# Performance work log

Hardware: AMD Instinct MI355X
Metric: run time of the kernel (lower is better)

The kernel has to match this reference:

```python
import jax, jax.numpy as jnp
import numpy as np

B, L, H, N = 8, 2048, 512, 64  # batch, seq_len, d_model, SSM state size


def setup_inputs() -> dict:
    key = jax.random.key(0)
    ks = jax.random.split(key, 10)
    x = jax.random.normal(ks[0], (B, L, H), jnp.float32)
    # S4D-style parameters (diagonal SSM, S4D-Lin init)
    log_dt = jnp.log(1e-3) + jax.random.uniform(ks[1], (H,), jnp.float32) * (jnp.log(1e-1) - jnp.log(1e-3))
    A_re = -0.5 * jnp.ones((H, N), jnp.float32)
    A_im = jnp.tile(np.pi * jnp.arange(N, dtype=np.float32), (H, 1))
    C_re = jax.random.normal(ks[2], (H, N), jnp.float32) * (0.5 ** 0.5)
    C_im = jax.random.normal(ks[3], (H, N), jnp.float32) * (0.5 ** 0.5)
    D_skip = jax.random.normal(ks[4], (H,), jnp.float32)
    # S4 output linear (GLU): d_model -> 2*d_model, then gated
    W_out = jax.random.normal(ks[5], (2 * H, H), jnp.float32) / np.sqrt(H)
    b_out = jnp.zeros((2 * H,), jnp.float32)
    # LayerNorms
    g1 = jnp.ones((H,), jnp.float32); beta1 = jnp.zeros((H,), jnp.float32)
    g2 = jnp.ones((H,), jnp.float32); beta2 = jnp.zeros((H,), jnp.float32)
    # 1x1 conv FFN (kernel_size=1 => pointwise linear), d_ff = d_model
    W1 = jax.random.normal(ks[6], (H, H), jnp.float32) / np.sqrt(H)
    bc1 = jnp.zeros((H,), jnp.float32)
    W2 = jax.random.normal(ks[7], (H, H), jnp.float32) / np.sqrt(H)
    bc2 = jnp.zeros((H,), jnp.float32)
    return dict(x=x, log_dt=log_dt, A_re=A_re, A_im=A_im, C_re=C_re, C_im=C_im,
                D_skip=D_skip, W_out=W_out, b_out=b_out, g1=g1, beta1=beta1,
                g2=g2, beta2=beta2, W1=W1, bc1=bc1, W2=W2, bc2=bc2)


def _layer_norm(x, g, b):
    mu = jnp.mean(x, axis=-1, keepdims=True)
    var = jnp.mean((x - mu) ** 2, axis=-1, keepdims=True)
    return (x - mu) / jnp.sqrt(var + 1e-5) * g + b


def _s4(x, log_dt, A_re, A_im, C_re, C_im, D_skip, W_out, b_out):
    # x: (B, L, H) channels-last (transposed=False)
    Lx = x.shape[1]
    dt = jnp.exp(log_dt)                       # (H,)
    A = A_re + 1j * A_im                       # (H, N) diagonal state matrix
    dtA = A * dt[:, None]
    # ZOH discretization of C: Ct = C * (exp(dt*A) - 1) / A
    Ct = (C_re + 1j * C_im) * ((jnp.exp(dtA) - 1.0) / A)
    # Vandermonde kernel: K[h, l] = 2 Re sum_n Ct[h,n] exp(dt*A[h,n]*l)
    l = jnp.arange(Lx, dtype=jnp.float32)
    K = 2.0 * jnp.real(jnp.einsum('hn,hnl->hl', Ct, jnp.exp(dtA[:, :, None] * l)))
    # FFT long convolution (linear conv via zero-padded circular conv)
    u = jnp.swapaxes(x, 1, 2)                  # (B, H, L)
    n = 2 * Lx
    y = jnp.fft.irfft(jnp.fft.rfft(u, n) * jnp.fft.rfft(K, n)[None], n)[..., :Lx]
    y = y + D_skip[None, :, None] * u          # skip connection D*u
    y = jax.nn.gelu(y)                         # S4 default activation
    # output linear + GLU (S4 default postact)
    z = jnp.einsum('bhl,fh->bfl', y, W_out) + b_out[None, :, None]
    a, g = jnp.split(z, 2, axis=1)
    y = a * jax.nn.sigmoid(g)
    return jnp.swapaxes(y, 1, 2)               # (B, L, H)


def reference(x, log_dt, A_re, A_im, C_re, C_im, D_skip, W_out, b_out,
              g1, beta1, g2, beta2, W1, bc1, W2, bc2):
    new_x = _s4(x, log_dt, A_re, A_im, C_re, C_im, D_skip, W_out, b_out)
    x = x + new_x
    x = _layer_norm(x, g1, beta1)
    # FFN via 1x1 convs (pointwise linears); dropout is identity in eval
    y = jax.nn.relu(jnp.einsum('blh,fh->blf', x, W1) + bc1)
    y = jnp.einsum('blf,hf->blh', y, W2) + bc2
    return _layer_norm(x + y, g2, beta2)
```

## Files before the change

kernel.cpp:

```cpp
#include <hip/hip_runtime.h>
#include <cstddef>
#include <cstdint>

#define B_DIM 8
#define L_DIM 2048
#define H_DIM 512
#define N_DIM 64
#define HN (H_DIM * N_DIM)
#define BLH (B_DIM * L_DIM * H_DIM)
#define M_DIM (B_DIM * L_DIM)

typedef unsigned short u16;
typedef short bf16x8 __attribute__((ext_vector_type(8)));
typedef float floatx4 __attribute__((ext_vector_type(4)));

__device__ __forceinline__ float sigmoidf_(float v) {
    return 1.0f / (1.0f + __expf(-v));
}

__device__ __forceinline__ float gelu_tanh_(float x) {
    float x3 = x * x * x;
    float z = 0.7978845608028654f * fmaf(0.044715f, x3, x);
    float e = __expf(-2.0f * fabsf(z));
    float th = (1.0f - e) / (1.0f + e);
    th = copysignf(th, z);
    return 0.5f * x * (1.0f + th);
}

__device__ __forceinline__ u16 f2b(float f) {
    unsigned u = __float_as_uint(f);
    unsigned r = (u + 0x7fffu + ((u >> 16) & 1u)) >> 16;
    return (u16)r;
}
__device__ __forceinline__ float b2f(u16 u) {
    return __uint_as_float(((unsigned)u) << 16);
}
__device__ __forceinline__ void unpack2(unsigned u, float& a, float& b) {
    a = __uint_as_float(u << 16);
    b = __uint_as_float(u & 0xffff0000u);
}
__device__ __forceinline__ unsigned pack2(float a, float b) {
    return (unsigned)f2b(a) | ((unsigned)f2b(b) << 16);
}

__device__ __forceinline__ void csq(float& r, float& i) {
    float nr = r * r - i * i;
    i = 2.0f * r * i;
    r = nr;
}

__global__ __launch_bounds__(256) void setup_kernel(
    const float* __restrict__ x, const float* __restrict__ W_out,
    const float* __restrict__ W1, const float* __restrict__ W2,
    const float* __restrict__ log_dt, const float* __restrict__ A_re,
    const float* __restrict__ A_im, const float* __restrict__ C_re,
    const float* __restrict__ C_im, const float* __restrict__ g1,
    const float* __restrict__ beta1,
    u16* __restrict__ XT, u16* __restrict__ Wobf, u16* __restrict__ W1gbf,
    u16* __restrict__ W2bf, float* __restrict__ P, u16* __restrict__ Toep_bf,
    float* __restrict__ c1, float* __restrict__ c2)
{
    __shared__ float tile[32][33];
    __shared__ float ktab_s[4][64];
    const int bid = blockIdx.x;
    const int t   = threadIdx.x;

    if (bid < 8192) {
        int b  = bid >> 10;
        int hy = (bid >> 6) & 15;
        int lx = bid & 63;
        int l0 = lx * 32, h0 = hy * 32;
        int tx = t & 31, ty = t >> 5;
        #pragma unroll
        for (int r = 0; r < 4; ++r)
            tile[ty + r * 8][tx] = x[((size_t)b * L_DIM + l0 + ty + r * 8) * H_DIM + h0 + tx];
        __syncthreads();
        #pragma unroll
        for (int r = 0; r < 4; ++r)
            XT[(((size_t)b * H_DIM + h0 + ty + r * 8) << 11) + l0 + tx] = f2b(tile[tx][ty + r * 8]);
    } else if (bid < 9216) {
        int off = bid - 8192;
        if (off < 512) {
            int i = off * 256 + t;
            float4 v = *(const float4*)(W_out + (size_t)i * 4);
            uint2 p; p.x = pack2(v.x, v.y); p.y = pack2(v.z, v.w);
            *(uint2*)(Wobf + (size_t)i * 4) = p;
        } else if (off < 768) {
            int i = (off - 512) * 256 + t;
            float4 v = *(const float4*)(W1 + (size_t)i * 4);
            int n = (i * 4) & 511;
            float4 g = *(const float4*)(g1 + n);
            uint2 p; p.x = pack2(v.x * g.x, v.y * g.y);
            p.y = pack2(v.z * g.z, v.w * g.w);
            *(uint2*)(W1gbf + (size_t)i * 4) = p;
        } else {
            int i = (off - 768) * 256 + t;
            float4 v = *(const float4*)(W2 + (size_t)i * 4);
            uint2 p; p.x = pack2(v.x, v.y); p.y = pack2(v.z, v.w);
            *(uint2*)(W2bf + (size_t)i * 4) = p;
        }
    } else if (bid < 9344) {
        const int wv = t >> 6, lane = t & 63;
        const int i = (bid - 9216) * 256 + t;
        const int h = i >> 6;
        float dt = expf(log_dt[h]);
        float Ar = A_re[i], Ai = A_im[i];
        float ar = dt * Ar, ai = dt * Ai;
        float e = expf(ar);
        float wr = e * cosf(ai);
        float wi = e * sinf(ai);
        float em1r = wr - 1.0f, em1i = wi;
        float inv = 1.0f / fmaf(Ar, Ar, Ai * Ai);
        float qr = fmaf(em1r, Ar, em1i * Ai) * inv;
        float qi = fmaf(em1i, Ar, -(em1r * Ai)) * inv;
        float Cr = C_re[i], Ci = C_im[i];
        float c2r = 2.0f * (Cr * qr - Ci * qi);
        float c2i = 2.0f * (Cr * qi + Ci * qr);
        P[i]          = wr;
        P[HN + i]     = wi;
        P[2 * HN + i] = c2r;
        P[3 * HN + i] = c2i;

        float pr = 1.0f, pi = 0.0f;
        for (int tau = 0; tau < 64; ++tau) {
            float term = c2r * pr - c2i * pi;
            #pragma unroll
            for (int m = 32; m > 0; m >>= 1) term += __shfl_xor(term, m, 64);
            if (lane == 0) ktab_s[wv][tau] = term;
            float nr = pr * wr - pi * wi, ni = pr * wi + pi * wr;
            pr = nr; pi = ni;
        }
        __syncthreads();

        const int h0 = (bid - 9216) * 4;
        #pragma unroll
        for (int r = 0; r < 8; ++r) {
            int c = t + r * 256;
            int hh = c >> 9, rem = c & 511;
            int tt = rem >> 3, j0 = (rem & 7) * 8;
            u16 vv[8];
            #pragma unroll
            for (int jj = 0; jj < 8; ++jj) {
                int j = j0 + jj;
                vv[jj] = (j <= tt) ? f2b(ktab_s[hh][tt - j]) : (u16)0;
            }
            *(uint4*)&Toep_bf[((size_t)(h0 + hh) << 12) + (tt << 6) + j0] = *(uint4*)vv;
        }
    } else {
        int f = (bid - 9344) * 4 + (t >> 6);
        int lane = t & 63;
        int n = lane * 8;
        float4 w0 = *(const float4*)(W1 + (size_t)f * 512 + n);
        float4 w1v = *(const float4*)(W1 + (size_t)f * 512 + n + 4);
        float4 ga = *(const float4*)(g1 + n);
        float4 gb = *(const float4*)(g1 + n + 4);
        float4 b0 = *(const float4*)(beta1 + n);
        float4 b1 = *(const float4*)(beta1 + n + 4);
        float s1 = w0.x * ga.x + w0.y * ga.y + w0.z * ga.z + w0.w * ga.w
                 + w1v.x * gb.x + w1v.y * gb.y + w1v.z * gb.z + w1v.w * gb.w;
        float s2 = w0.x * b0.x + w0.y * b0.y + w0.z * b0.z + w0.w * b0.w
                 + w1v.x * b1.x + w1v.y * b1.y + w1v.z * b1.z + w1v.w * b1.w;
        #pragma unroll
        for (int m = 32; m > 0; m >>= 1) {
            s1 += __shfl_xor(s1, m, 64);
            s2 += __shfl_xor(s2, m, 64);
        }
        if (lane == 0) { c1[f] = s1; c2[f] = s2; }
    }
}

__global__ __launch_bounds__(256) void ssm_chunk_kernel(
    const u16* __restrict__ XT, const float* __restrict__ P,
    const u16* __restrict__ Toep_bf, const float* __restrict__ D_skip,
    u16* __restrict__ YT)
{
    __shared__ u16 U[128 * 72];
    __shared__ u16 S[128 * 136];
    __shared__ u16 EVT[13312];
    u16* E  = EVT;
    u16* Tp = EVT;
    u16* V  = EVT + 4608;

    const int h    = blockIdx.x;
    const int b0   = blockIdx.y * 4;
    const int t    = threadIdx.x;
    const int lane = t & 63;
    const int wv   = t >> 6;
    const int lm   = lane & 15, lq = lane >> 4;

    const int pidx = (h << 6) + lane;
    const float wr  = P[pidx],          wi  = P[HN + pidx];
    const float c2r = P[2 * HN + pidx], c2i = P[3 * HN + pidx];

    #pragma unroll
    for (int r = 0; r < 4; ++r) {
        int idx = t + r * 256;
        int row = idx >> 3, ch = idx & 7;
        const u16* gp = XT + (((size_t)(b0 + (row >> 5)) * H_DIM + h) << 11)
                           + ((row & 31) << 6) + (ch << 3);
        *(uint4*)&U[row * 72 + ch * 8] = *(const uint4*)gp;
    }

    float bwr, bwi;
    {
        float g16r = wr, g16i = wi;
        csq(g16r, g16i); csq(g16r, g16i); csq(g16r, g16i); csq(g16r, g16i);
        if (wv == 0)      { bwr = 1.0f; bwi = 0.0f; }
        else if (wv == 1) { bwr = g16r; bwi = g16i; }
        else if (wv == 2) { bwr = g16r; bwi = g16i; csq(bwr, bwi); }
        else {
            float g32r = g16r, g32i = g16i; csq(g32r, g32i);
            bwr = g32r * g16r - g32i * g16i;
            bwi = g32r * g16i + g32i * g16r;
        }
    }

    {
        float pr = bwr, pi = bwi;
        #pragma unroll
        for (int jk = 0; jk < 16; ++jk) {
            int k = (wv << 4) + jk;
            int j = 63 - k;
            E[(2 * lane) * 72 + j]     = f2b(pr);
            E[(2 * lane + 1) * 72 + j] = f2b(pi);
            float nr = pr * wr - pi * wi, ni = pr * wi + pi * wr;
            pr = nr; pi = ni;
        }
    }
    __syncthreads();

    {
        const int wm = wv >> 1, wn = wv & 1;
        floatx4 acc[4][4] = {};
        #pragma unroll
        for (int ks = 0; ks < 2; ++ks) {
            bf16x8 af[4], bfv[4];
            #pragma unroll
            for (int i = 0; i < 4; ++i)
                af[i] = *(const bf16x8*)&E[(wm * 64 + i * 16 + lm) * 72 + ks * 32 + lq * 8];
            #pragma unroll
            for (int j = 0; j < 4; ++j)
                bfv[j] = *(const bf16x8*)&U[(wn * 64 + j * 16 + lm) * 72 + ks * 32 + lq * 8];
            #pragma unroll
            for (int i = 0; i < 4; ++i) {
                #pragma unroll
                for (int j = 0; j < 4; ++j)
                    acc[i][j] = __builtin_amdgcn_mfma_f32_16x16x32_bf16(af[i], bfv[j], acc[i][j], 0, 0, 0);
            }
        }
        #pragma unroll
        for (int i = 0; i < 4; ++i) {
            #pragma unroll
            for (int j = 0; j < 4; ++j) {
                int ncol = wn * 64 + j * 16 + lm;
                int m0   = wm * 64 + i * 16 + lq * 4;
                u16 pk[4];
                #pragma unroll
                for (int r = 0; r < 4; ++r) pk[r] = f2b(acc[i][j][r]);
                *(uint2*)&S[ncol * 136 + m0] = *(uint2*)pk;
            }
        }
    }
    __syncthreads();

    {
        float pr = bwr, pi = bwi;
        {
            float nr = pr * wr - pi * wi, ni = pr * wi + pi * wr;
            pr = nr; pi = ni;
        }
        #pragma unroll
        for (int jk = 1; jk <= 16; ++jk) {
            int tr = (wv << 4) + jk - 1;
            float qr = c2r * pr - c2i * pi;
            float qi = c2r * pi + c2i * pr;
            V[tr * 136 + 2 * lane]     = f2b(qr);
            V[tr * 136 + 2 * lane + 1] = f2b(-qi);
            float nr = pr * wr - pi * wi, ni = pr * wi + pi * wr;
            pr = nr; pi = ni;
        }
        #pragma unroll
        for (int r = 0; r < 2; ++r) {
            int idx = t + r * 256;
            int row = idx >> 3, ch = idx & 7;
            *(uint4*)&Tp[row * 72 + ch * 8] =
                *(const uint4*)&Toep_bf[((size_t)h << 12) + (row << 6) + (ch << 3)];
        }
        float wTr = wr, wTi = wi;
        csq(wTr, wTi); csq(wTr, wTi); csq(wTr, wTi);
        csq(wTr, wTi); csq(wTr, wTi); csq(wTr, wTi);
        float Sr = 0.0f, Si = 0.0f;
        const int n2 = lane * 2;
        for (int c = 0; c < 32; ++c) {
            int base = (wv * 32 + c) * 136 + n2;
            unsigned lv = *(unsigned*)&S[base];
            float lr, li;
            unpack2(lv, lr, li);
            *(unsigned*)&S[base] = pack2(Sr, Si);
            float nSr = wTr * Sr - wTi * Si + lr;
            Si = wTr * Si + wTi * Sr + li;
            Sr = nSr;
        }
    }
    __syncthreads();

    {
        const float Dh = D_skip[h];
        floatx4 acc[4][2] = {};
        #pragma unroll
        for (int ks = 0; ks < 6; ++ks) {
            bf16x8 af[4], bfv[2];
            if (ks < 2) {
                #pragma unroll
                for (int i = 0; i < 4; ++i)
                    af[i] = *(const bf16x8*)&Tp[(i * 16 + lm) * 72 + ks * 32 + lq * 8];
                #pragma unroll
                for (int j = 0; j < 2; ++j)
                    bfv[j] = *(const bf16x8*)&U[(wv * 32 + j * 16 + lm) * 72 + ks * 32 + lq * 8];
            } else {
                #pragma unroll
                for (int i = 0; i < 4; ++i)
                    af[i] = *(const bf16x8*)&V[(i * 16 + lm) * 136 + (ks - 2) * 32 + lq * 8];
                #pragma unroll
                for (int j = 0; j < 2; ++j)
                    bfv[j] = *(const bf16x8*)&S[(wv * 32 + j * 16 + lm) * 136 + (ks - 2) * 32 + lq * 8];
            }
            #pragma unroll
            for (int i = 0; i < 4; ++i) {
                #pragma unroll
                for (int j = 0; j < 2; ++j)
                    acc[i][j] = __builtin_amdgcn_mfma_f32_16x16x32_bf16(af[i], bfv[j], acc[i][j], 0, 0, 0);
            }
        }
        #pragma unroll
        for (int j = 0; j < 2; ++j) {
            int ncol = wv * 32 + j * 16 + lm;
            int bloc = ncol >> 5, c = ncol & 31;
            size_t gbase = (((size_t)(b0 + bloc) * H_DIM + h) << 11) + (c << 6);
            #pragma unroll
            for (int i = 0; i < 4; ++i) {
                int t0 = i * 16 + lq * 4;
                u16 upk[4];
                *(uint2*)upk = *(const uint2*)&U[ncol * 72 + t0];
                u16 opk[4];
                #pragma unroll
                for (int r = 0; r < 4; ++r) {
                    float uvv = b2f(upk[r]);
                    float yv = gelu_tanh_(fmaf(Dh, uvv, acc[i][j][r]));
                    opk[r] = f2b(yv);
                }
                *(uint2*)&YT[gbase + t0] = *(uint2*)opk;
            }
        }
    }
}

__device__ __forceinline__ void stage_tile_512(
    const u16* __restrict__ g, u16* lds, int row0, int k0)
{
    const int t = threadIdx.x;
    const int row  = t >> 2;
    const int csrc = (t & 3) ^ ((t >> 3) & 3);
    const u16* gp = g + (size_t)(row0 + row) * 512 + k0 + csrc * 8;
    __builtin_amdgcn_global_load_lds(
        (const __attribute__((address_space(1))) unsigned int*)gp,
        (__attribute__((address_space(3))) unsigned int*)(lds + (size_t)t * 8),
        16, 0, 0);
}

__device__ __forceinline__ void stage_tile64_512(
    const u16* __restrict__ g, u16* lds, int row0, int k0)
{
    const int t = threadIdx.x;
    #pragma unroll
    for (int r = 0; r < 2; ++r) {
        int c   = t + r * 512;
        int row = c >> 3, cc = c & 7;
        int csrc = cc ^ (row & 7);
        const u16* gp = g + (size_t)(row0 + row) * 512 + k0 + csrc * 8;
        __builtin_amdgcn_global_load_lds(
            (const __attribute__((address_space(1))) unsigned int*)gp,
            (__attribute__((address_space(3))) unsigned int*)(lds + (size_t)c * 8),
            16, 0, 0);
    }
}

__device__ __forceinline__ uint4 ldA_yt(
    const u16* __restrict__ YT, int b, int l0, int k0)
{
    const int k  = threadIdx.x >> 4;
    const int lc = threadIdx.x & 15;
    return *(const uint4*)(YT + (((size_t)(b * 512 + k0 + k)) << 11) + l0 + lc * 8);
}
__device__ __forceinline__ void dswA(u16* lds, uint4 av)
{
    const int k  = threadIdx.x >> 4;
    const int lc = threadIdx.x & 15;
    u16* p = lds + (lc * 8) * 32 + (((k >> 3) ^ (lc & 3)) << 3) + (k & 7);
    const u16* s = (const u16*)&av;
    #pragma unroll
    for (int j = 0; j < 8; ++j) p[j * 32] = s[j];
}

__global__ __launch_bounds__(512) void gemm1_glu_kernel(
    const u16* __restrict__ YT, const u16* __restrict__ Wo,
    const float* __restrict__ bo, const float* __restrict__ x,
    u16* __restrict__ out, float2* __restrict__ Pstats)
{
    __shared__ u16 As[2][128 * 32];
    __shared__ u16 Ba[2][128 * 32];
    __shared__ u16 Bg[2][128 * 32];
    __shared__ float2 red1[128][4];
    const int t    = threadIdx.x;
    const int lane = t & 63;
    const int wv   = t >> 6;
    const int wm   = wv >> 2, wn = wv & 3;
    const int lm   = lane & 15, lq = lane >> 4;
    const int sw   = (lq ^ ((lm >> 1) & 3)) * 8;
    const int m0   = blockIdx.x * 128, n0 = blockIdx.y * 128;
    const int b    = m0 >> 11;
    const int l0   = m0 & 2047;
    floatx4 accA[4][2] = {};
    floatx4 accG[4][2] = {};

    int swA[4];
    #pragma unroll
    for (int i = 0; i < 4; ++i)
        swA[i] = (lq ^ ((i * 2 + (lm >> 3)) & 3)) * 8;

    uint4 av = ldA_yt(YT, b, l0, 0);
    stage_tile_512(Wo, Ba[0], n0, 0);
    stage_tile_512(Wo, Bg[0], 512 + n0, 0);
    dswA(As[0], av);
    __syncthreads();

    int cur = 0;
    for (int k0 = 32; k0 < 512; k0 += 32) {
        const int nx = cur ^ 1;
        uint4 avn = ldA_yt(YT, b, l0, k0);
        stage_tile_512(Wo, Ba[nx], n0, k0);
        stage_tile_512(Wo, Bg[nx], 512 + n0, k0);

        bf16x8 af[4], ba[2], bg[2];
        #pragma unroll
        for (int i = 0; i < 4; ++i)
            af[i] = *(const bf16x8*)&As[cur][(wm * 64 + i * 16 + lm) * 32 + swA[i]];
        #pragma unroll
        for (int j = 0; j < 2; ++j) {
            ba[j] = *(const bf16x8*)&Ba[cur][(wn * 32 + j * 16 + lm) * 32 + sw];
            bg[j] = *(const bf16x8*)&Bg[cur][(wn * 32 + j * 16 + lm) * 32 + sw];
        }
        #pragma unroll
        for (int i = 0; i < 4; ++i) {
            #pragma unroll
            for (int j = 0; j < 2; ++j) {
                accA[i][j] = __builtin_amdgcn_mfma_f32_16x16x32_bf16(af[i], ba[j], accA[i][j], 0, 0, 0);
                accG[i][j] = __builtin_amdgcn_mfma_f32_16x16x32_bf16(af[i], bg[j], accG[i][j], 0, 0, 0);
            }
        }
        dswA(As[nx], avn);
        __syncthreads();
        cur = nx;
    }
    {
        bf16x8 af[4], ba[2], bg[2];
        #pragma unroll
        for (int i = 0; i < 4; ++i)
            af[i] = *(const bf16x8*)&As[cur][(wm * 64 + i * 16 + lm) * 32 + swA[i]];
        #pragma unroll
        for (int j = 0; j < 2; ++j) {
            ba[j] = *(const bf16x8*)&Ba[cur][(wn * 32 + j * 16 + lm) * 32 + sw];
            bg[j] = *(const bf16x8*)&Bg[cur][(wn * 32 + j * 16 + lm) * 32 + sw];
        }
        #pragma unroll
        for (int i = 0; i < 4; ++i) {
            #pragma unroll
            for (int j = 0; j < 2; ++j) {
                accA[i][j] = __builtin_amdgcn_mfma_f32_16x16x32_bf16(af[i], ba[j], accA[i][j], 0, 0, 0);
                accG[i][j] = __builtin_amdgcn_mfma_f32_16x16x32_bf16(af[i], bg[j], accG[i][j], 0, 0, 0);
            }
        }
    }

    float bav[2], bgv[2];
    #pragma unroll
    for (int j = 0; j < 2; ++j) {
        int n = n0 + wn * 32 + j * 16 + lm;
        bav[j] = bo[n]; bgv[j] = bo[512 + n];
    }
    #pragma unroll
    for (int i = 0; i < 4; ++i) {
        #pragma unroll
        for (int r = 0; r < 4; ++r) {
            int row = wm * 64 + i * 16 + lq * 4 + r;
            int m = m0 + row;
            float s = 0.0f, sq = 0.0f;
            #pragma unroll
            for (int j = 0; j < 2; ++j) {
                int n = n0 + wn * 32 + j * 16 + lm;
                float a_ = accA[i][j][r] + bav[j];
                float g_ = accG[i][j][r] + bgv[j];
                float xv = x[(size_t)m * 512 + n];
                float ov = fmaf(a_, sigmoidf_(g_), xv);
                out[(size_t)m * 512 + n] = f2b(ov);
                s += ov; sq = fmaf(ov, ov, sq);
            }
            #pragma unroll
            for (int msk = 1; msk < 16; msk <<= 1) {
                s  += __shfl_xor(s, msk, 64);
                sq += __shfl_xor(sq, msk, 64);
            }
            if (lm == 0) { float2 p; p.x = s; p.y = sq; red1[row][wn] = p; }
        }
    }
    __syncthreads();
    if (t < 128) {
        float s = 0.0f, sq = 0.0f;
        #pragma unroll
        for (int w = 0; w < 4; ++w) { float2 p = red1[t][w]; s += p.x; sq += p.y; }
        float2 o; o.x = s; o.y = sq;
        Pstats[(size_t)(m0 + t) * 4 + blockIdx.y] = o;
    }
}

__global__ __launch_bounds__(512, 4) void gemm_relu_kernel(
    const u16* __restrict__ A, const u16* __restrict__ Bw,
    const float* __restrict__ bias, const float2* __restrict__ Pstats,
    const float* __restrict__ c1, const float* __restrict__ c2,
    u16* __restrict__ C)
{
    __shared__ u16 As[2][128 * 64];
    __shared__ u16 Bs[2][128 * 64];
    __shared__ float musig[128][2];
    const int t    = threadIdx.x;
    const int lane = t & 63;
    const int wv   = t >> 6;
    const int wm   = wv >> 2, wn = wv & 3;
    const int lm   = lane & 15, lq = lane >> 4;
    const int kc0  = (lq ^ (lm & 7)) * 8;
    const int kc1  = ((4 + lq) ^ (lm & 7)) * 8;
    const int m0   = blockIdx.x * 128, n0 = blockIdx.y * 128;
    floatx4 acc[4][2] = {};

    if (t < 128) {
        float s = 0.0f, sq = 0.0f;
        #pragma unroll
        for (int w = 0; w < 4; ++w) {
            float2 p = Pstats[(size_t)(m0 + t) * 4 + w];
            s += p.x; sq += p.y;
        }
        float mu  = s * (1.0f / 512.0f);
        float var = sq * (1.0f / 512.0f) - mu * mu;
        musig[t][0] = mu;
        musig[t][1] = rsqrtf(var + 1e-5f);
    }
    stage_tile64_512(A, As[0], m0, 0);
    stage_tile64_512(Bw, Bs[0], n0, 0);
    __syncthreads();

    int cur = 0;
    for (int k0 = 64; k0 < 512; k0 += 64) {
        const int nx = cur ^ 1;
        stage_tile64_512(A, As[nx], m0, k0);
        stage_tile64_512(Bw, Bs[nx], n0, k0);

        #pragma unroll
        for (int ks = 0; ks < 2; ++ks) {
            const int kc = ks ? kc1 : kc0;
            bf16x8 af[4], bfr[2];
            #pragma unroll
            for (int i = 0; i < 4; ++i)
                af[i] = *(const bf16x8*)&As[cur][(wm * 64 + i * 16 + lm) * 64 + kc];
            #pragma unroll
            for (int j = 0; j < 2; ++j)
                bfr[j] = *(const bf16x8*)&Bs[cur][(wn * 32 + j * 16 + lm) * 64 + kc];
            #pragma unroll
            for (int i = 0; i < 4; ++i) {
                #pragma unroll
                for (int j = 0; j < 2; ++j)
                    acc[i][j] = __builtin_amdgcn_mfma_f32_16x16x32_bf16(af[i], bfr[j], acc[i][j], 0, 0, 0);
            }
        }
        __syncthreads();
        cur = nx;
    }
    #pragma unroll
    for (int ks = 0; ks < 2; ++ks) {
        const int kc = ks ? kc1 : kc0;
        bf16x8 af[4], bfr[2];
        #pragma unroll
        for (int i = 0; i < 4; ++i)
            af[i] = *(const bf16x8*)&As[cur][(wm * 64 + i * 16 + lm) * 64 + kc];
        #pragma unroll
        for (int j = 0; j < 2; ++j)
            bfr[j] = *(const bf16x8*)&Bs[cur][(wn * 32 + j * 16 + lm) * 64 + kc];
        #pragma unroll
        for (int i = 0; i < 4; ++i) {
            #pragma unroll
            for (int j = 0; j < 2; ++j)
                acc[i][j] = __builtin_amdgcn_mfma_f32_16x16x32_bf16(af[i], bfr[j], acc[i][j], 0, 0, 0);
        }
    }
    float c1v[2], c2v[2];
    #pragma unroll
    for (int j = 0; j < 2; ++j) {
        int n = n0 + wn * 32 + j * 16 + lm;
        c1v[j] = c1[n];
        c2v[j] = c2[n] + bias[n];
    }
    #pragma unroll
    for (int i = 0; i < 4; ++i) {
        #pragma unroll
        for (int r = 0; r < 4; ++r) {
            int row = wm * 64 + i * 16 + lq * 4 + r;
            float mu = musig[row][0], rs = musig[row][1];
            float nmr = -rs * mu;
            #pragma unroll
            for (int j = 0; j < 2; ++j) {
                int n = n0 + wn * 32 + j * 16 + lm;
                float v = fmaf(rs, acc[i][j][r], fmaf(nmr, c1v[j], c2v[j]));
                C[(size_t)(m0 + row) * 512 + n] = f2b(fmaxf(v, 0.0f));
            }
        }
    }
}

__global__ __launch_bounds__(512, 4) void gemm2_tile_kernel(
    const u16* __restrict__ A, const u16* __restrict__ Bw,
    const float* __restrict__ bias, const u16* __restrict__ res,
    const float2* __restrict__ Pstats,
    const float* __restrict__ g1, const float* __restrict__ beta1,
    u16* __restrict__ Z, float2* __restrict__ Pstats2)
{
    __shared__ u16 As[2][128 * 64];
    __shared__ u16 Bs[2][128 * 64];
    __shared__ float musig[128][2];
    __shared__ float2 red2[128][4];
    const int t    = threadIdx.x;
    const int lane = t & 63;
    const int wv   = t >> 6;
    const int wm   = wv >> 2, wn = wv & 3;
    const int lm   = lane & 15, lq = lane >> 4;
    const int kc0  = (lq ^ (lm & 7)) * 8;
    const int kc1  = ((4 + lq) ^ (lm & 7)) * 8;
    const int m0   = blockIdx.x * 128, n0 = blockIdx.y * 128;
    floatx4 acc[4][2] = {};

    if (t < 128) {
        float s = 0.0f, sq = 0.0f;
        #pragma unroll
        for (int w = 0; w < 4; ++w) {
            float2 p = Pstats[(size_t)(m0 + t) * 4 + w];
            s += p.x; sq += p.y;
        }
        float mu  = s * (1.0f / 512.0f);
        float var = sq * (1.0f / 512.0f) - mu * mu;
        musig[t][0] = mu;
        musig[t][1] = rsqrtf(var + 1e-5f);
    }
    stage_tile64_512(A, As[0], m0, 0);
    stage_tile64_512(Bw, Bs[0], n0, 0);
    __syncthreads();

    int cur = 0;
    for (int k0 = 64; k0 < 512; k0 += 64) {
        const int nx = cur ^ 1;
        stage_tile64_512(A, As[nx], m0, k0);
        stage_tile64_512(Bw, Bs[nx], n0, k0);

        #pragma unroll
        for (int ks = 0; ks < 2; ++ks) {
            const int kc = ks ? kc1 : kc0;
            bf16x8 af[4], bfr[2];
            #pragma unroll
            for (int i = 0; i < 4; ++i)
                af[i] = *(const bf16x8*)&As[cur][(wm * 64 + i * 16 + lm) * 64 + kc];
            #pragma unroll
            for (int j = 0; j < 2; ++j)
                bfr[j] = *(const bf16x8*)&Bs[cur][(wn * 32 + j * 16 + lm) * 64 + kc];
            #pragma unroll
            for (int i = 0; i < 4; ++i) {
                #pragma unroll
                for (int j = 0; j < 2; ++j)
                    acc[i][j] = __builtin_amdgcn_mfma_f32_16x16x32_bf16(af[i], bfr[j], acc[i][j], 0, 0, 0);
            }
        }
        __syncthreads();
        cur = nx;
    }
    #pragma unroll
    for (int ks = 0; ks < 2; ++ks) {
        const int kc = ks ? kc1 : kc0;
        bf16x8 af[4], bfr[2];
        #pragma unroll
        for (int i = 0; i < 4; ++i)
            af[i] = *(const bf16x8*)&As[cur][(wm * 64 + i * 16 + lm) * 64 + kc];
        #pragma unroll
        for (int j = 0; j < 2; ++j)
            bfr[j] = *(const bf16x8*)&Bs[cur][(wn * 32 + j * 16 + lm) * 64 + kc];
        #pragma unroll
        for (int i = 0; i < 4; ++i) {
            #pragma unroll
            for (int j = 0; j < 2; ++j)
                acc[i][j] = __builtin_amdgcn_mfma_f32_16x16x32_bf16(af[i], bfr[j], acc[i][j], 0, 0, 0);
        }
    }

    float bv[2], gv1[2], bt1[2];
    #pragma unroll
    for (int j = 0; j < 2; ++j) {
        int n = n0 + wn * 32 + j * 16 + lm;
        bv[j]  = bias[n];
        gv1[j] = g1[n];
        bt1[j] = beta1[n];
    }
    #pragma unroll
    for (int i = 0; i < 4; ++i) {
        #pragma unroll
        for (int r = 0; r < 4; ++r) {
            int row = wm * 64 + i * 16 + lq * 4 + r;
            int m = m0 + row;
            float mu1 = musig[row][0], rs1 = musig[row][1];
            float s = 0.0f, sq = 0.0f;
            #pragma unroll
            for (int j = 0; j < 2; ++j) {
                int n = n0 + wn * 32 + j * 16 + lm;
                float zl = fmaf((b2f(res[(size_t)m * 512 + n]) - mu1) * rs1, gv1[j], bt1[j]);
                float v = acc[i][j][r] + bv[j] + zl;
                Z[(size_t)m * 512 + n] = f2b(v);
                s += v; sq = fmaf(v, v, sq);
            }
            #pragma unroll
            for (int msk = 1; msk < 16; msk <<= 1) {
                s  += __shfl_xor(s, msk, 64);
                sq += __shfl_xor(sq, msk, 64);
            }
            if (lm == 0) { float2 p; p.x = s; p.y = sq; red2[row][wn] = p; }
        }
    }
    __syncthreads();
    if (t < 128) {
        float s = 0.0f, sq = 0.0f;
        #pragma unroll
        for (int w = 0; w < 4; ++w) { float2 p = red2[t][w]; s += p.x; sq += p.y; }
        float2 o; o.x = s; o.y = sq;
        Pstats2[(size_t)(m0 + t) * 4 + blockIdx.y] = o;
    }
}

__global__ __launch_bounds__(256) void ln2_finish_kernel(
    const u16* __restrict__ Z, const float2* __restrict__ Pstats2,
    const float* __restrict__ gamma, const float* __restrict__ beta,
    float* __restrict__ out)
{
    int w    = threadIdx.x >> 6;
    int lane = threadIdx.x & 63;
    size_t row  = (size_t)blockIdx.x * 4 + w;
    float s = 0.0f, sq = 0.0f;
    #pragma unroll
    for (int w4 = 0; w4 < 4; ++w4) {
        float2 p = Pstats2[row * 4 + w4];
        s += p.x; sq += p.y;
    }
    float mu  = s * (1.0f / 512.0f);
    float var = sq * (1.0f / 512.0f) - mu * mu;
    float rs  = rsqrtf(var + 1e-5f);
    size_t base = row * 512 + lane * 8;
    uint4 raw = *(const uint4*)(Z + base);
    float v[8];
    unpack2(raw.x, v[0], v[1]); unpack2(raw.y, v[2], v[3]);
    unpack2(raw.z, v[4], v[5]); unpack2(raw.w, v[6], v[7]);
    float g[8], bt[8];
    *(float4*)&g[0]  = *(const float4*)(gamma + lane * 8);
    *(float4*)&g[4]  = *(const float4*)(gamma + lane * 8 + 4);
    *(float4*)&bt[0] = *(const float4*)(beta + lane * 8);
    *(float4*)&bt[4] = *(const float4*)(beta + lane * 8 + 4);
    float o[8];
    #pragma unroll
    for (int i = 0; i < 8; ++i)
        o[i] = fmaf((v[i] - mu) * rs, g[i], bt[i]);
    *(float4*)(out + base)     = *(float4*)&o[0];
    *(float4*)(out + base + 4) = *(float4*)&o[4];
}

extern "C" void kernel_launch(void* const* d_in, const int* in_sizes, int n_in,
                              void* d_out, int out_size, void* d_ws, size_t ws_size,
                              hipStream_t stream)
{
    (void)in_sizes; (void)n_in; (void)out_size; (void)ws_size;
    const float* x      = (const float*)d_in[0];
    const float* log_dt = (const float*)d_in[1];
    const float* A_re   = (const float*)d_in[2];
    const float* A_im   = (const float*)d_in[3];
    const float* C_re   = (const float*)d_in[4];
    const float* C_im   = (const float*)d_in[5];
    const float* D_skip = (const float*)d_in[6];
    const float* W_out  = (const float*)d_in[7];
    const float* b_out  = (const float*)d_in[8];
    const float* g1     = (const float*)d_in[9];
    const float* beta1  = (const float*)d_in[10];
    const float* g2     = (const float*)d_in[11];
    const float* beta2  = (const float*)d_in[12];
    const float* W1     = (const float*)d_in[13];
    const float* bc1    = (const float*)d_in[14];
    const float* W2     = (const float*)d_in[15];
    const float* bc2    = (const float*)d_in[16];
    float* out = (float*)d_out;

    char*   wsb    = (char*)d_ws;
    float*  P      = (float*)wsb;
    u16*    Toep   = (u16*)(wsb + 4 * HN * 4 + 512 * 64 * 4);
    u16*    Wobf   = Toep + 512 * 4096;
    u16*    W1bf   = Wobf + 1024 * 512;
    u16*    W2bf   = W1bf + 512 * 512;
    u16*    r1     = W2bf + 512 * 512;
    u16*    r2     = r1 + BLH;
    u16*    r3     = r2 + BLH;
    float2* Pstats = (float2*)(r3 + BLH);
    float*  c1     = (float*)(Pstats + (size_t)M_DIM * 4);
    float*  c2     = c1 + 512;
    float2* Pstats2 = (float2*)(c2 + 512);

    setup_kernel<<<9472, 256, 0, stream>>>(x, W_out, W1, W2, log_dt, A_re, A_im,
                                           C_re, C_im, g1, beta1,
                                           r1, Wobf, W1bf, W2bf, P, Toep, c1, c2);
    ssm_chunk_kernel<<<dim3(H_DIM, 2), 256, 0, stream>>>(r1, P, Toep, D_skip, r2);
    gemm1_glu_kernel<<<dim3(M_DIM / 128, 4), 512, 0, stream>>>(r2, Wobf, b_out, x, r3, Pstats);
    gemm_relu_kernel<<<dim3(M_DIM / 128, 4), 512, 0, stream>>>(r3, W1bf, bc1, Pstats, c1, c2, r1);
    gemm2_tile_kernel<<<dim3(M_DIM / 128, 4), 512, 0, stream>>>(r1, W2bf, bc2, r3, Pstats, g1, beta1, r2, Pstats2);
    ln2_finish_kernel<<<M_DIM / 4, 256, 0, stream>>>(r2, Pstats2, g2, beta2, out);
}
```

Measured before the change: 234.5 us.

## Prefetch two K-tiles ahead in FFN GEMMs with explicit vmcnt waits

Reworks the K loop of the two LayerNorm-fused FFN GEMM kernels so that two stages are in flight. Each iteration waits only on the older stage's global loads (vmcnt(4)) and then refills that buffer with the tile two steps ahead. It uses raw s_barrier plus sched_barrier in place of __syncthreads, aiming to hide global-load latency behind the MFMA work. This depends on stage_tile64_512 issuing exactly the assumed number of loads (likely direct-to-LDS), and an incorrect vmcnt count would race.

```diff
diff --git a/kernel.cpp b/kernel.cpp
--- a/kernel.cpp
+++ b/kernel.cpp
@@ -554,16 +554,19 @@
         musig[t][0] = mu;
         musig[t][1] = rsqrtf(var + 1e-5f);
     }
-    stage_tile64_512(A, As[0], m0, 0);
+    asm volatile("s_waitcnt vmcnt(0)" ::: "memory");
+
+    stage_tile64_512(A,  As[0], m0, 0);
     stage_tile64_512(Bw, Bs[0], n0, 0);
-    __syncthreads();
-
-    int cur = 0;
-    for (int k0 = 64; k0 < 512; k0 += 64) {
-        const int nx = cur ^ 1;
-        stage_tile64_512(A, As[nx], m0, k0);
-        stage_tile64_512(Bw, Bs[nx], n0, k0);
-
+    stage_tile64_512(A,  As[1], m0, 64);
+    stage_tile64_512(Bw, Bs[1], n0, 64);
+
+    #pragma unroll 1
+    for (int it = 0; it < 7; ++it) {
+        asm volatile("s_waitcnt vmcnt(4)" ::: "memory");
+        __builtin_amdgcn_s_barrier();
+        __builtin_amdgcn_sched_barrier(0);
+        const int cur = it & 1;
         #pragma unroll
         for (int ks = 0; ks < 2; ++ks) {
             const int kc = ks ? kc1 : kc0;
@@ -581,19 +584,26 @@
                     acc[i][j] = __builtin_amdgcn_mfma_f32_16x16x32_bf16(af[i], bfr[j], acc[i][j], 0, 0, 0);
             }
         }
-        __syncthreads();
-        cur = nx;
-    }
+        __builtin_amdgcn_s_barrier();
+        __builtin_amdgcn_sched_barrier(0);
+        if (it < 6) {
+            stage_tile64_512(A,  As[cur], m0, (it + 2) * 64);
+            stage_tile64_512(Bw, Bs[cur], n0, (it + 2) * 64);
+        }
+    }
+    asm volatile("s_waitcnt vmcnt(0)" ::: "memory");
+    __builtin_amdgcn_s_barrier();
+    __builtin_amdgcn_sched_barrier(0);
     #pragma unroll
     for (int ks = 0; ks < 2; ++ks) {
         const int kc = ks ? kc1 : kc0;
         bf16x8 af[4], bfr[2];
         #pragma unroll
         for (int i = 0; i < 4; ++i)
-            af[i] = *(const bf16x8*)&As[cur][(wm * 64 + i * 16 + lm) * 64 + kc];
+            af[i] = *(const bf16x8*)&As[1][(wm * 64 + i * 16 + lm) * 64 + kc];
         #pragma unroll
         for (int j = 0; j < 2; ++j)
-            bfr[j] = *(const bf16x8*)&Bs[cur][(wn * 32 + j * 16 + lm) * 64 + kc];
+            bfr[j] = *(const bf16x8*)&Bs[1][(wn * 32 + j * 16 + lm) * 64 + kc];
         #pragma unroll
         for (int i = 0; i < 4; ++i) {
             #pragma unroll
@@ -658,16 +668,19 @@
         musig[t][0] = mu;
         musig[t][1] = rsqrtf(var + 1e-5f);
     }
-    stage_tile64_512(A, As[0], m0, 0);
+    asm volatile("s_waitcnt vmcnt(0)" ::: "memory");
+
+    stage_tile64_512(A,  As[0], m0, 0);
     stage_tile64_512(Bw, Bs[0], n0, 0);
-    __syncthreads();
-
-    int cur = 0;
-    for (int k0 = 64; k0 < 512; k0 += 64) {
-        const int nx = cur ^ 1;
-        stage_tile64_512(A, As[nx], m0, k0);
-        stage_tile64_512(Bw, Bs[nx], n0, k0);
-
+    stage_tile64_512(A,  As[1], m0, 64);
+    stage_tile64_512(Bw, Bs[1], n0, 64);
+
+    #pragma unroll 1
+    for (int it = 0; it < 7; ++it) {
+        asm volatile("s_waitcnt vmcnt(4)" ::: "memory");
+        __builtin_amdgcn_s_barrier();
+        __builtin_amdgcn_sched_barrier(0);
+        const int cur = it & 1;
         #pragma unroll
         for (int ks = 0; ks < 2; ++ks) {
             const int kc = ks ? kc1 : kc0;
@@ -685,19 +698,26 @@
                     acc[i][j] = __builtin_amdgcn_mfma_f32_16x16x32_bf16(af[i], bfr[j], acc[i][j], 0, 0, 0);
             }
         }
-        __syncthreads();
-        cur = nx;
-    }
+        __builtin_amdgcn_s_barrier();
+        __builtin_amdgcn_sched_barrier(0);
+        if (it < 6) {
+            stage_tile64_512(A,  As[cur], m0, (it + 2) * 64);
+            stage_tile64_512(Bw, Bs[cur], n0, (it + 2) * 64);
+        }
+    }
+    asm volatile("s_waitcnt vmcnt(0)" ::: "memory");
+    __builtin_amdgcn_s_barrier();
+    __builtin_amdgcn_sched_barrier(0);
     #pragma unroll
     for (int ks = 0; ks < 2; ++ks) {
         const int kc = ks ? kc1 : kc0;
         bf16x8 af[4], bfr[2];
         #pragma unroll
         for (int i = 0; i < 4; ++i)
-            af[i] = *(const bf16x8*)&As[cur][(wm * 64 + i * 16 + lm) * 64 + kc];
+            af[i] = *(const bf16x8*)&As[1][(wm * 64 + i * 16 + lm) * 64 + kc];
         #pragma unroll
         for (int j = 0; j < 2; ++j)
-            bfr[j] = *(const bf16x8*)&Bs[cur][(wn * 32 + j * 16 + lm) * 64 + kc];
+            bfr[j] = *(const bf16x8*)&Bs[1][(wn * 32 + j * 16 + lm) * 64 + kc];
         #pragma unroll
         for (int i = 0; i < 4; ++i) {
             #pragma unroll
```

New measurement: 231.9 us. No clear change (-1.1%).
